# Kernel optimization log

Measured on AMD Instinct MI355X. Metric: run time of the kernel, lower is better.

## Reference

```python
import jax, jax.numpy as jnp
import numpy as np

B, T, C = 2, 192, 512
H, D = 8, 64  # num_heads, head_dim; inner_dim = H*D = C


def setup_inputs() -> dict:
    key = jax.random.key(0)
    k1, k2, k3 = jax.random.split(key, 3)
    x = jax.random.normal(k1, (B, T, C), dtype=jnp.float32)
    W_in = jax.random.normal(k2, (C, 5 * H * D), dtype=jnp.float32) * 0.02
    b_in = jnp.zeros((5 * H * D,), dtype=jnp.float32)
    W_out = jax.random.normal(k3, (H * D, C), dtype=jnp.float32) * 0.02
    b_out = jnp.zeros((C,), dtype=jnp.float32)
    return {"x": x, "W_in": W_in, "b_in": b_in, "W_out": W_out, "b_out": b_out}


def _split_heads(t):
    # (B,T,H*D) -> (B,H,T,D)
    return t.reshape(B, T, H, D).transpose(0, 2, 1, 3)


def reference(x, W_in, b_in, W_out, b_out):
    scale = D ** -0.5
    proj = x @ W_in + b_in  # (B,T,5*H*D)
    q, k1, v1, k2, v2 = jnp.split(proj, 5, axis=-1)
    q = _split_heads(q) * scale
    k1 = _split_heads(k1)
    v1 = _split_heads(v1)
    k2 = _split_heads(k2)
    v2 = _split_heads(v2)
    # trilinear logits: <q_i, k1_j, k2_k> / sqrt(D), computed in fp32
    logits = jnp.einsum('bhid,bhjd,bhkd->bhijk', q, k1, k2,
                        preferred_element_type=jnp.float32)
    # softmax over the joint (j,k) axes
    attn = jax.nn.softmax(logits.reshape(B, H, T, T * T), axis=-1)
    attn = attn.reshape(B, H, T, T, T).astype(x.dtype)
    # out_i[d] = sum_{j,k} attn[i,j,k] * v1_j[d] * v2_k[d]
    out = jnp.einsum('bhijk,bhjd,bhkd->bhid', attn, v1, v2)
    y = out.transpose(0, 2, 1, 3).reshape(B, T, H * D)  # merge heads
    return y @ W_out + b_out
```

## Files before the change

kernel.cpp:

```cpp
#include <hip/hip_runtime.h>
#include <hip/hip_bf16.h>


typedef float  v4f __attribute__((ext_vector_type(4)));
typedef short  v8s __attribute__((ext_vector_type(8)));

__device__ __forceinline__ unsigned short f2bf(float f) {
  unsigned u = __float_as_uint(f);
  u += 0x7fffu + ((u >> 16) & 1u);
  return (unsigned short)(u >> 16);
}
__device__ __forceinline__ float bf2f(unsigned short b) {
  return __uint_as_float(((unsigned)b) << 16);
}
__device__ __forceinline__ unsigned pack_bf16(float lo, float hi) {
  __hip_bfloat162 t = __float22bfloat162_rn(float2{lo, hi});
  union { __hip_bfloat162 b; unsigned u; } cv;
  cv.b = t;
  return cv.u;
}

#if __has_builtin(__builtin_amdgcn_exp2f)
#define EXP2F(x) __builtin_amdgcn_exp2f(x)
#else
#define EXP2F(x) exp2f(x)
#endif

#define MFMA32(a, b, c) __builtin_amdgcn_mfma_f32_16x16x32_bf16((a), (b), (c), 0, 0, 0)

#define QSCALE 0.18033688011112042f


#define XH_OFF   589824
#define XL_OFF   786432
#define WTH_OFF  983040
#define WTL_OFF  2293760
#define WOTH_OFF 3604480
#define WOTL_OFF 3866624
#define OH_OFF   4128768
#define OL_OFF   4325376

__device__ __forceinline__ int v1perm(int t) {
  const int h = (t >= 96) ? 1 : 0;
  const int jh = t - 96 * h;
  const int jtl = jh >> 4, rem = jh & 15;
  const int m = jtl >> 1;
  const int w = ((jtl & 1) << 1) | ((rem >> 1) & 1);
  const int k = ((rem >> 2) << 3) | (w << 1) | (rem & 1);
  return h * 96 + m * 32 + k;
}

__global__ __launch_bounds__(256) void prep_kernel(
    const float* __restrict__ x, const float* __restrict__ Win,
    const float* __restrict__ Wout, unsigned short* __restrict__ wsh) {
  __shared__ float tile[32 * 65];
  const int bi = blockIdx.x, t = threadIdx.x;
  if (bi < 768) {
    const float* W; unsigned short *Th, *Tl; int R, n0, k0;
    if (bi < 640) {
      W = Win; Th = wsh + WTH_OFF; Tl = wsh + WTL_OFF; R = 2560;
      n0 = (bi % 40) << 6; k0 = (bi / 40) << 5;
    } else {
      const int idx = bi - 640;
      W = Wout; Th = wsh + WOTH_OFF; Tl = wsh + WOTL_OFF; R = 512;
      n0 = (idx & 7) << 6; k0 = (idx >> 3) << 5;
    }
    const int n = t & 63, kq = (t >> 6) * 8;
#pragma unroll
    for (int j = 0; j < 8; ++j)
      tile[(kq + j) * 65 + n] = W[(k0 + kq + j) * R + n0 + n];
    __syncthreads();
    const int n2 = t >> 2, ks = (t & 3) * 8;
    union { uint4 u; unsigned short us[8]; } ph, pl;
#pragma unroll
    for (int j = 0; j < 8; ++j) {
      const float v = tile[(ks + j) * 65 + n2];
      const unsigned short h = f2bf(v);
      ph.us[j] = h;
      pl.us[j] = f2bf(v - bf2f(h));
    }
    *(uint4*)(Th + (n0 + n2) * 512 + k0 + ks) = ph.u;
    *(uint4*)(Tl + (n0 + n2) * 512 + k0 + ks) = pl.u;
  } else {
    const int flat = ((bi - 768) * 256 + t) * 8;
    const v4f v0 = *(const v4f*)(x + flat);
    const v4f v1 = *(const v4f*)(x + flat + 4);
    union { uint4 u; unsigned short us[8]; } ph, pl;
#pragma unroll
    for (int j = 0; j < 4; ++j) {
      unsigned short h = f2bf(v0[j]);
      ph.us[j] = h; pl.us[j] = f2bf(v0[j] - bf2f(h));
      h = f2bf(v1[j]);
      ph.us[4 + j] = h; pl.us[4 + j] = f2bf(v1[j] - bf2f(h));
    }
    *(uint4*)(wsh + XH_OFF + flat) = ph.u;
    *(uint4*)(wsh + XL_OFF + flat) = pl.u;
  }
}

__global__ __launch_bounds__(256) void proj_kernel(
    const unsigned short* __restrict__ wsh, const float* __restrict__ bin,
    float* __restrict__ wsf, unsigned short* __restrict__ wshd) {
  __shared__ float red[4][32][33];
  const int tid = threadIdx.x;
  const int wv = tid >> 6, lane = tid & 63;
  const int c = lane & 15, q = lane >> 4;
  const int bm = blockIdx.x, bn = blockIdx.y;
  const int k0 = wv * 128;

  const unsigned short* base[8];
  base[0] = wsh + XH_OFF + (bm * 32 + c) * 512 + (q << 3) + k0;
  base[1] = base[0] + 16 * 512;
  base[2] = wsh + XL_OFF + (bm * 32 + c) * 512 + (q << 3) + k0;
  base[3] = base[2] + 16 * 512;
  base[4] = wsh + WTH_OFF + (bn * 32 + c) * 512 + (q << 3) + k0;
  base[5] = base[4] + 16 * 512;
  base[6] = wsh + WTL_OFF + (bn * 32 + c) * 512 + (q << 3) + k0;
  base[7] = base[6] + 16 * 512;

  const v4f z = {0.f, 0.f, 0.f, 0.f};
  v4f a00 = z, a01 = z, a10 = z, a11 = z;

  v8s cur[8], nxt[8];
#pragma unroll
  for (int i = 0; i < 8; ++i) cur[i] = *(const v8s*)(base[i]);
#pragma unroll 1
  for (int ks = 0; ks < 4; ++ks) {
    if (ks < 3) {
      const int o = (ks + 1) * 32;
#pragma unroll
      for (int i = 0; i < 8; ++i) nxt[i] = *(const v8s*)(base[i] + o);
    }
    a00 = MFMA32(cur[2], cur[4], a00); a00 = MFMA32(cur[0], cur[6], a00); a00 = MFMA32(cur[0], cur[4], a00);
    a01 = MFMA32(cur[2], cur[5], a01); a01 = MFMA32(cur[0], cur[7], a01); a01 = MFMA32(cur[0], cur[5], a01);
    a10 = MFMA32(cur[3], cur[4], a10); a10 = MFMA32(cur[1], cur[6], a10); a10 = MFMA32(cur[1], cur[4], a10);
    a11 = MFMA32(cur[3], cur[5], a11); a11 = MFMA32(cur[1], cur[7], a11); a11 = MFMA32(cur[1], cur[5], a11);
#pragma unroll
    for (int i = 0; i < 8; ++i) cur[i] = nxt[i];
  }

  v4f accs[2][2] = {{a00, a01}, {a10, a11}};
#pragma unroll
  for (int mt = 0; mt < 2; ++mt)
#pragma unroll
    for (int nt = 0; nt < 2; ++nt)
#pragma unroll
      for (int r = 0; r < 4; ++r)
        red[wv][mt * 16 + (q << 2) + r][nt * 16 + c] = accs[mt][nt][r];
  __syncthreads();

#pragma unroll
  for (int j = 0; j < 4; ++j) {
    const int o = tid + (j << 8);
    const int row = o >> 5, col = o & 31;
    const int n = bn * 32 + col;
    const float val = red[0][row][col] + red[1][row][col] +
                      red[2][row][col] + red[3][row][col] + bin[n];
    const int m = bm * 32 + row;
    const int which = n >> 9, cc = n & 511, hh = cc >> 6, d = cc & 63;
    const int b = (m >= 192) ? 1 : 0;
    const int tt = m - (b ? 192 : 0);
    const int bh = b * 8 + hh;
    const int rm = ((bh * 192 + tt) << 6) + d;
    if (which == 0)      wsf[rm] = val * QSCALE;
    else if (which == 1) wshd[rm] = f2bf(val);
    else if (which == 2) wshd[393216 + ((bh << 6) + d) * 192 + v1perm(tt)] = f2bf(val);
    else if (which == 3) wshd[196608 + rm] = f2bf(val);
    else wsf[196608 + ((bh * 192 + tt) * 16 + (d & 15)) * 4 + (d >> 4)] = val;
  }
}

__global__ __launch_bounds__(256, 2) void attn_kernel(
    const float* __restrict__ wsf, const unsigned short* __restrict__ wsh,
    float* __restrict__ accp, float* __restrict__ Sp) {
  __shared__ unsigned short smem[25600];
  unsigned short* V1s = smem;
  unsigned short* K1s = smem + 12544;

  const int tid  = threadIdx.x;
  const int wv   = tid >> 6;
  const int lane = tid & 63;
  const int c    = lane & 15;
  const int quad = lane >> 4;

  const int bb = blockIdx.x;
  const int kb = bb & 3;
  const int it = (bb >> 2) % 12;
  const int bh = bb / 48;

  const unsigned short* k1g = wsh + bh * 192 * 64;
  const unsigned short* v1g = wsh + 393216 + bh * 64 * 192;
  const unsigned short* k2g = wsh + 196608 + bh * 192 * 64;
  const float*          v2g = wsf + 196608 + bh * 12288;

  for (int idx = tid; idx < 3072; idx += 256) {
    if (idx < 1536) {
      const int r = idx / 24, c8 = (idx % 24) * 8;
      *(uint4*)(V1s + r * 196 + c8) = *(const uint4*)(v1g + r * 192 + c8);
    } else {
      const int j = idx - 1536;
      const int r = j >> 3, c8 = (j & 7) << 3;
      *(uint4*)(K1s + r * 68 + c8) = *(const uint4*)(k1g + (r << 6) + c8);
    }
  }

  const float* qg = wsf + ((bh * 192 + it * 16 + c) << 6) + (quad << 3);
  float q0[8], q1[8];
  {
    v4f qa = *(const v4f*)(qg), qb = *(const v4f*)(qg + 4);
    v4f qc = *(const v4f*)(qg + 32), qd = *(const v4f*)(qg + 36);
#pragma unroll
    for (int e = 0; e < 4; ++e) {
      q0[e] = qa[e]; q0[4 + e] = qb[e];
      q1[e] = qc[e]; q1[4 + e] = qd[e];
    }
  }
  __syncthreads();

  const v4f z = {0.f, 0.f, 0.f, 0.f};
  v4f acc[4] = {z, z, z, z};
  v4f oS = z;
  const short one = (short)0x3F80;
  const v8s ones = {one, one, one, one, one, one, one, one};

  const int kstart = kb * 48 + wv * 12;
  union U4 { uint4 u4; unsigned short us[8]; };
  union AF { v8s v; unsigned u[4]; };

  U4 kl, kh, nkl, nkh;
  kl.u4 = *(const uint4*)(k2g + (kstart << 6) + (quad << 3));
  kh.u4 = *(const uint4*)(k2g + (kstart << 6) + (quad << 3) + 32);
  v4f v2 = *(const v4f*)(v2g + (kstart << 6) + (c << 2));

#pragma unroll 1
  for (int s = 0; s < 12; ++s) {
    v4f nv2;
    if (s < 11) {
      const int o = ((kstart + s + 1) << 6);
      nkl.u4 = *(const uint4*)(k2g + o + (quad << 3));
      nkh.u4 = *(const uint4*)(k2g + o + (quad << 3) + 32);
      nv2 = *(const v4f*)(v2g + o + (c << 2));
    }

    AF af0, af1;
#pragma unroll
    for (int e = 0; e < 4; ++e) {
      af0.u[e] = pack_bf16(q0[2*e] * bf2f(kl.us[2*e]), q0[2*e+1] * bf2f(kl.us[2*e+1]));
      af1.u[e] = pack_bf16(q1[2*e] * bf2f(kh.us[2*e]), q1[2*e+1] * bf2f(kh.us[2*e+1]));
    }

    v4f o[4] = {z, z, z, z};
#pragma unroll
    for (int h = 0; h < 2; ++h) {
      v4f C[6];
#pragma unroll
      for (int j6 = 0; j6 < 6; ++j6) {
        const unsigned short* kp = K1s + ((h * 6 + j6) * 16 + c) * 68 + (quad << 3);
        v4f t0 = MFMA32(*(const v8s*)kp, af0.v, z);
        C[j6] = MFMA32(*(const v8s*)(kp + 32), af1.v, t0);
      }
#pragma unroll
      for (int j6 = 0; j6 < 6; ++j6)
#pragma unroll
        for (int r = 0; r < 4; ++r) C[j6][r] = EXP2F(C[j6][r]);
      AF p[3];
#pragma unroll
      for (int m = 0; m < 3; ++m)
#pragma unroll
        for (int w = 0; w < 4; ++w) {
          const int jt = 2 * m + (w >> 1), r0 = (w & 1) * 2;
          p[m].u[w] = pack_bf16(C[jt][r0], C[jt][r0 + 1]);
        }
#pragma unroll
      for (int m = 0; m < 3; ++m) {
        oS = MFMA32(p[m].v, ones, oS);
        const int vcol = (h * 3 + m) * 32 + (quad << 3);
#pragma unroll
        for (int t = 0; t < 4; ++t) {
          const v8s vf = *(const v8s*)(V1s + (c + 16 * t) * 196 + vcol);
          o[t] = MFMA32(p[m].v, vf, o[t]);
        }
      }
    }
#pragma unroll
    for (int t = 0; t < 4; ++t) acc[t] += o[t] * v2[t];
    kl = nkl; kh = nkh; v2 = nv2;
  }

  __syncthreads();
  float* redA = (float*)smem;
  float* redS = (float*)smem + 4096;

  if (c == 0) {
    float* rs = redS + wv * 16 + (quad << 2);
#pragma unroll
    for (int r = 0; r < 4; ++r) rs[r] = oS[r];
  }
#pragma unroll
  for (int r = 0; r < 4; ++r) {
    float* rr = redA + wv * 1024 + (((quad << 2) + r) << 6) + c;
    rr[0] = acc[0][r]; rr[16] = acc[1][r]; rr[32] = acc[2][r]; rr[48] = acc[3][r];
  }
  __syncthreads();

  const int pbase = (bh * 12 + it) * 4 + kb;
  float* ap_out = accp + pbase * 1024;
  for (int idx = tid; idx < 1024; idx += 256)
    ap_out[idx] = redA[idx] + redA[1024 + idx] + redA[2048 + idx] + redA[3072 + idx];
  if (tid < 16)
    Sp[pbase * 16 + tid] = redS[tid] + redS[16 + tid] + redS[32 + tid] + redS[48 + tid];
}

__global__ __launch_bounds__(256) void norm_kernel(
    const float* __restrict__ accp, const float* __restrict__ Sp,
    unsigned short* __restrict__ wsh) {
  const int flat = blockIdx.x * 2048 + threadIdx.x * 8;
  const int m = flat >> 9, cc = flat & 511;
  const int b = (m >= 192) ? 1 : 0;
  const int tt = m - (b ? 192 : 0);
  const int h = cc >> 6, d0 = cc & 63;
  const int bh = b * 8 + h, it = tt >> 4, i = tt & 15;
  const int pb = (bh * 12 + it) * 4;
  const float* ap = accp + pb * 1024 + (i << 6) + d0;
  v4f a0 = *(const v4f*)(ap), a1 = *(const v4f*)(ap + 4);
  float Sv = Sp[pb * 16 + i];
#pragma unroll
  for (int kb = 1; kb < 4; ++kb) {
    a0 += *(const v4f*)(ap + kb * 1024);
    a1 += *(const v4f*)(ap + kb * 1024 + 4);
    Sv += Sp[(pb + kb) * 16 + i];
  }
  const float inv = 1.0f / Sv;
  union { uint4 u; unsigned short us[8]; } ph, pl;
#pragma unroll
  for (int j = 0; j < 4; ++j) {
    float v = a0[j] * inv;
    unsigned short hh = f2bf(v);
    ph.us[j] = hh; pl.us[j] = f2bf(v - bf2f(hh));
    v = a1[j] * inv;
    hh = f2bf(v);
    ph.us[4 + j] = hh; pl.us[4 + j] = f2bf(v - bf2f(hh));
  }
  *(uint4*)(wsh + OH_OFF + flat) = ph.u;
  *(uint4*)(wsh + OL_OFF + flat) = pl.u;
}

__global__ __launch_bounds__(256) void outp_kernel(
    const unsigned short* __restrict__ wsh, const float* __restrict__ bout,
    float* __restrict__ y) {
  __shared__ float red[4][32][33];
  const int tid = threadIdx.x;
  const int wv = tid >> 6, lane = tid & 63;
  const int c = lane & 15, q = lane >> 4;
  const int bm = blockIdx.x, bn = blockIdx.y;
  const int k0 = wv * 128;

  const unsigned short* base[8];
  base[0] = wsh + OH_OFF + (bm * 32 + c) * 512 + (q << 3) + k0;
  base[1] = base[0] + 16 * 512;
  base[2] = wsh + OL_OFF + (bm * 32 + c) * 512 + (q << 3) + k0;
  base[3] = base[2] + 16 * 512;
  base[4] = wsh + WOTH_OFF + (bn * 32 + c) * 512 + (q << 3) + k0;
  base[5] = base[4] + 16 * 512;
  base[6] = wsh + WOTL_OFF + (bn * 32 + c) * 512 + (q << 3) + k0;
  base[7] = base[6] + 16 * 512;

  const v4f z = {0.f, 0.f, 0.f, 0.f};
  v4f a00 = z, a01 = z, a10 = z, a11 = z;

  v8s cur[8], nxt[8];
#pragma unroll
  for (int i = 0; i < 8; ++i) cur[i] = *(const v8s*)(base[i]);
#pragma unroll 1
  for (int ks = 0; ks < 4; ++ks) {
    if (ks < 3) {
      const int o = (ks + 1) * 32;
#pragma unroll
      for (int i = 0; i < 8; ++i) nxt[i] = *(const v8s*)(base[i] + o);
    }
    a00 = MFMA32(cur[2], cur[4], a00); a00 = MFMA32(cur[0], cur[6], a00); a00 = MFMA32(cur[0], cur[4], a00);
    a01 = MFMA32(cur[2], cur[5], a01); a01 = MFMA32(cur[0], cur[7], a01); a01 = MFMA32(cur[0], cur[5], a01);
    a10 = MFMA32(cur[3], cur[4], a10); a10 = MFMA32(cur[1], cur[6], a10); a10 = MFMA32(cur[1], cur[4], a10);
    a11 = MFMA32(cur[3], cur[5], a11); a11 = MFMA32(cur[1], cur[7], a11); a11 = MFMA32(cur[1], cur[5], a11);
#pragma unroll
    for (int i = 0; i < 8; ++i) cur[i] = nxt[i];
  }

  v4f accs[2][2] = {{a00, a01}, {a10, a11}};
#pragma unroll
  for (int mt = 0; mt < 2; ++mt)
#pragma unroll
    for (int nt = 0; nt < 2; ++nt)
#pragma unroll
      for (int r = 0; r < 4; ++r)
        red[wv][mt * 16 + (q << 2) + r][nt * 16 + c] = accs[mt][nt][r];
  __syncthreads();

#pragma unroll
  for (int j = 0; j < 4; ++j) {
    const int o = tid + (j << 8);
    const int row = o >> 5, col = o & 31;
    const int n = bn * 32 + col;
    const float val = red[0][row][col] + red[1][row][col] +
                      red[2][row][col] + red[3][row][col] + bout[n];
    y[(bm * 32 + row) * 512 + n] = val;
  }
}

extern "C" void kernel_launch(void* const* d_in, const int* in_sizes, int n_in,
                              void* d_out, int out_size, void* d_ws, size_t ws_size,
                              hipStream_t stream) {
  const float* x    = (const float*)d_in[0];
  const float* Win  = (const float*)d_in[1];
  const float* bin  = (const float*)d_in[2];
  const float* Wout = (const float*)d_in[3];
  const float* bout = (const float*)d_in[4];

  float* wsf = (float*)d_ws;
  unsigned short* wsh = (unsigned short*)(wsf + 1191936);
  float* accp = wsf + 393216;
  float* Sp   = wsf + 1179648;

  prep_kernel<<<dim3(864), 256, 0, stream>>>(x, Win, Wout, wsh);
  proj_kernel<<<dim3(12, 80), 256, 0, stream>>>(wsh, bin, wsf, wsh);
  attn_kernel<<<dim3(768), 256, 0, stream>>>(wsf, wsh, accp, Sp);
  norm_kernel<<<dim3(96), 256, 0, stream>>>(accp, Sp, wsh);
  outp_kernel<<<dim3(12, 16), 256, 0, stream>>>(wsh, bout, (float*)d_out);
}
```

Measured before the change: 174.6 us.

## Fuse normalization into output projection and compute softmax sum with VALU adds

Removes the norm kernel: the output projection now reduces the four partial accumulators, divides by the summed softmax denominator and splits into bf16 hi/lo fragments directly in its GEMM loop. In the attention kernel, the row-sum MFMA against a ones vector is replaced by scalar float accumulation of the exponentials plus cross-lane shuffles. The attention kernel's launch bound minimum-blocks hint is lowered from 2 to 1, giving the compiler more register room. The fused projection recomputes the normalization for each output-column block and loses its explicit software prefetch.

```diff
diff --git a/kernel.cpp b/kernel.cpp
--- a/kernel.cpp
+++ b/kernel.cpp
@@ -37,8 +37,6 @@
 #define WTL_OFF  2293760
 #define WOTH_OFF 3604480
 #define WOTL_OFF 3866624
-#define OH_OFF   4128768
-#define OL_OFF   4325376
 
 __device__ __forceinline__ int v1perm(int t) {
   const int h = (t >= 96) ? 1 : 0;
@@ -170,7 +168,7 @@
   }
 }
 
-__global__ __launch_bounds__(256, 2) void attn_kernel(
+__global__ __launch_bounds__(256, 1) void attn_kernel(
     const float* __restrict__ wsf, const unsigned short* __restrict__ wsh,
     float* __restrict__ accp, float* __restrict__ Sp) {
   __shared__ unsigned short smem[25600];
@@ -219,9 +217,7 @@
 
   const v4f z = {0.f, 0.f, 0.f, 0.f};
   v4f acc[4] = {z, z, z, z};
-  v4f oS = z;
-  const short one = (short)0x3F80;
-  const v8s ones = {one, one, one, one, one, one, one, one};
+  float sS = 0.f;
 
   const int kstart = kb * 48 + wv * 12;
   union U4 { uint4 u4; unsigned short us[8]; };
@@ -262,7 +258,10 @@
 #pragma unroll
       for (int j6 = 0; j6 < 6; ++j6)
 #pragma unroll
-        for (int r = 0; r < 4; ++r) C[j6][r] = EXP2F(C[j6][r]);
+        for (int r = 0; r < 4; ++r) {
+          C[j6][r] = EXP2F(C[j6][r]);
+          sS += C[j6][r];
+        }
       AF p[3];
 #pragma unroll
       for (int m = 0; m < 3; ++m)
@@ -273,7 +272,6 @@
         }
 #pragma unroll
       for (int m = 0; m < 3; ++m) {
-        oS = MFMA32(p[m].v, ones, oS);
         const int vcol = (h * 3 + m) * 32 + (quad << 3);
 #pragma unroll
         for (int t = 0; t < 4; ++t) {
@@ -291,11 +289,9 @@
   float* redA = (float*)smem;
   float* redS = (float*)smem + 4096;
 
-  if (c == 0) {
-    float* rs = redS + wv * 16 + (quad << 2);
-#pragma unroll
-    for (int r = 0; r < 4; ++r) rs[r] = oS[r];
-  }
+  sS += __shfl_xor(sS, 16, 64);
+  sS += __shfl_xor(sS, 32, 64);
+  if (quad == 0) redS[wv * 16 + c] = sS;
 #pragma unroll
   for (int r = 0; r < 4; ++r) {
     float* rr = redA + wv * 1024 + (((quad << 2) + r) << 6) + c;
@@ -311,41 +307,8 @@
     Sp[pbase * 16 + tid] = redS[tid] + redS[16 + tid] + redS[32 + tid] + redS[48 + tid];
 }
 
-__global__ __launch_bounds__(256) void norm_kernel(
+__global__ __launch_bounds__(256) void outp_kernel(
     const float* __restrict__ accp, const float* __restrict__ Sp,
-    unsigned short* __restrict__ wsh) {
-  const int flat = blockIdx.x * 2048 + threadIdx.x * 8;
-  const int m = flat >> 9, cc = flat & 511;
-  const int b = (m >= 192) ? 1 : 0;
-  const int tt = m - (b ? 192 : 0);
-  const int h = cc >> 6, d0 = cc & 63;
-  const int bh = b * 8 + h, it = tt >> 4, i = tt & 15;
-  const int pb = (bh * 12 + it) * 4;
-  const float* ap = accp + pb * 1024 + (i << 6) + d0;
-  v4f a0 = *(const v4f*)(ap), a1 = *(const v4f*)(ap + 4);
-  float Sv = Sp[pb * 16 + i];
-#pragma unroll
-  for (int kb = 1; kb < 4; ++kb) {
-    a0 += *(const v4f*)(ap + kb * 1024);
-    a1 += *(const v4f*)(ap + kb * 1024 + 4);
-    Sv += Sp[(pb + kb) * 16 + i];
-  }
-  const float inv = 1.0f / Sv;
-  union { uint4 u; unsigned short us[8]; } ph, pl;
-#pragma unroll
-  for (int j = 0; j < 4; ++j) {
-    float v = a0[j] * inv;
-    unsigned short hh = f2bf(v);
-    ph.us[j] = hh; pl.us[j] = f2bf(v - bf2f(hh));
-    v = a1[j] * inv;
-    hh = f2bf(v);
-    ph.us[4 + j] = hh; pl.us[4 + j] = f2bf(v - bf2f(hh));
-  }
-  *(uint4*)(wsh + OH_OFF + flat) = ph.u;
-  *(uint4*)(wsh + OL_OFF + flat) = pl.u;
-}
-
-__global__ __launch_bounds__(256) void outp_kernel(
     const unsigned short* __restrict__ wsh, const float* __restrict__ bout,
     float* __restrict__ y) {
   __shared__ float red[4][32][33];
@@ -355,35 +318,65 @@
   const int bm = blockIdx.x, bn = blockIdx.y;
   const int k0 = wv * 128;
 
-  const unsigned short* base[8];
-  base[0] = wsh + OH_OFF + (bm * 32 + c) * 512 + (q << 3) + k0;
-  base[1] = base[0] + 16 * 512;
-  base[2] = wsh + OL_OFF + (bm * 32 + c) * 512 + (q << 3) + k0;
-  base[3] = base[2] + 16 * 512;
-  base[4] = wsh + WOTH_OFF + (bn * 32 + c) * 512 + (q << 3) + k0;
-  base[5] = base[4] + 16 * 512;
-  base[6] = wsh + WOTL_OFF + (bn * 32 + c) * 512 + (q << 3) + k0;
-  base[7] = base[6] + 16 * 512;
+  int pbase_[2][2];
+  float inv_[2][2];
+#pragma unroll
+  for (int mt = 0; mt < 2; ++mt) {
+    const int m = bm * 32 + mt * 16 + c;
+    const int b = (m >= 192) ? 1 : 0;
+    const int t = m - (b ? 192 : 0);
+    const int it = t >> 4, i = t & 15;
+#pragma unroll
+    for (int hh = 0; hh < 2; ++hh) {
+      const int bh = b * 8 + wv * 2 + hh;
+      const int pb = (bh * 12 + it) * 4;
+      pbase_[mt][hh] = pb * 1024 + (i << 6);
+      const float Sv = Sp[pb * 16 + i] + Sp[(pb + 1) * 16 + i] +
+                       Sp[(pb + 2) * 16 + i] + Sp[(pb + 3) * 16 + i];
+      inv_[mt][hh] = 1.0f / Sv;
+    }
+  }
+
+  const unsigned short* bh0 = wsh + WOTH_OFF + (bn * 32 + c) * 512 + (q << 3) + k0;
+  const unsigned short* bh1 = bh0 + 16 * 512;
+  const unsigned short* bl0 = wsh + WOTL_OFF + (bn * 32 + c) * 512 + (q << 3) + k0;
+  const unsigned short* bl1 = bl0 + 16 * 512;
 
   const v4f z = {0.f, 0.f, 0.f, 0.f};
   v4f a00 = z, a01 = z, a10 = z, a11 = z;
 
-  v8s cur[8], nxt[8];
-#pragma unroll
-  for (int i = 0; i < 8; ++i) cur[i] = *(const v8s*)(base[i]);
-#pragma unroll 1
+#pragma unroll
   for (int ks = 0; ks < 4; ++ks) {
-    if (ks < 3) {
-      const int o = (ks + 1) * 32;
-#pragma unroll
-      for (int i = 0; i < 8; ++i) nxt[i] = *(const v8s*)(base[i] + o);
-    }
-    a00 = MFMA32(cur[2], cur[4], a00); a00 = MFMA32(cur[0], cur[6], a00); a00 = MFMA32(cur[0], cur[4], a00);
-    a01 = MFMA32(cur[2], cur[5], a01); a01 = MFMA32(cur[0], cur[7], a01); a01 = MFMA32(cur[0], cur[5], a01);
-    a10 = MFMA32(cur[3], cur[4], a10); a10 = MFMA32(cur[1], cur[6], a10); a10 = MFMA32(cur[1], cur[4], a10);
-    a11 = MFMA32(cur[3], cur[5], a11); a11 = MFMA32(cur[1], cur[7], a11); a11 = MFMA32(cur[1], cur[5], a11);
-#pragma unroll
-    for (int i = 0; i < 8; ++i) cur[i] = nxt[i];
+    const int hh = ks >> 1;
+    const int d0 = (ks & 1) * 32 + (q << 3);
+    v8s Ah[2], Al[2];
+#pragma unroll
+    for (int mt = 0; mt < 2; ++mt) {
+      const float* ap = accp + pbase_[mt][hh] + d0;
+      v4f s0 = *(const v4f*)(ap) + *(const v4f*)(ap + 1024) +
+               *(const v4f*)(ap + 2048) + *(const v4f*)(ap + 3072);
+      v4f s1 = *(const v4f*)(ap + 4) + *(const v4f*)(ap + 1028) +
+               *(const v4f*)(ap + 2052) + *(const v4f*)(ap + 3076);
+      const float iv = inv_[mt][hh];
+      union { v8s v; unsigned short us[8]; } hfr, lfr;
+#pragma unroll
+      for (int e = 0; e < 4; ++e) {
+        float v0 = s0[e] * iv;
+        unsigned short hb = f2bf(v0);
+        hfr.us[e] = hb; lfr.us[e] = f2bf(v0 - bf2f(hb));
+        float v1 = s1[e] * iv;
+        hb = f2bf(v1);
+        hfr.us[4 + e] = hb; lfr.us[4 + e] = f2bf(v1 - bf2f(hb));
+      }
+      Ah[mt] = hfr.v; Al[mt] = lfr.v;
+    }
+    const int o = ks * 32;
+    const v8s Bh0 = *(const v8s*)(bh0 + o), Bh1 = *(const v8s*)(bh1 + o);
+    const v8s Bl0 = *(const v8s*)(bl0 + o), Bl1 = *(const v8s*)(bl1 + o);
+    a00 = MFMA32(Al[0], Bh0, a00); a00 = MFMA32(Ah[0], Bl0, a00); a00 = MFMA32(Ah[0], Bh0, a00);
+    a01 = MFMA32(Al[0], Bh1, a01); a01 = MFMA32(Ah[0], Bl1, a01); a01 = MFMA32(Ah[0], Bh1, a01);
+    a10 = MFMA32(Al[1], Bh0, a10); a10 = MFMA32(Ah[1], Bl0, a10); a10 = MFMA32(Ah[1], Bh0, a10);
+    a11 = MFMA32(Al[1], Bh1, a11); a11 = MFMA32(Ah[1], Bl1, a11); a11 = MFMA32(Ah[1], Bh1, a11);
   }
 
   v4f accs[2][2] = {{a00, a01}, {a10, a11}};
@@ -424,6 +417,5 @@
   prep_kernel<<<dim3(864), 256, 0, stream>>>(x, Win, Wout, wsh);
   proj_kernel<<<dim3(12, 80), 256, 0, stream>>>(wsh, bin, wsf, wsh);
   attn_kernel<<<dim3(768), 256, 0, stream>>>(wsf, wsh, accp, Sp);
-  norm_kernel<<<dim3(96), 256, 0, stream>>>(accp, Sp, wsh);
-  outp_kernel<<<dim3(12, 16), 256, 0, stream>>>(wsh, bout, (float*)d_out);
-}
+  outp_kernel<<<dim3(12, 16), 256, 0, stream>>>(accp, Sp, wsh, bout, (float*)d_out);
+}
```

Measured after the change: 174.4 us. Within noise of the previous version (-0.1%).
